# Kernel optimization log

Measured on AMD Instinct MI355X. Metric: run time of the kernel, lower is better.

The kernel has to match this reference:

```python
import jax, jax.numpy as jnp
import numpy as np

ALPHA = 0.2  # LeakyReLU negative slope
NEG_INF = -9e15


def setup_inputs() -> dict:
    key = jax.random.key(0)
    k1, k2, k3, k4, k5 = jax.random.split(key, 5)
    B, N, F_in, F_out = 1, 8192, 256, 128
    h = jax.random.normal(k1, (B, N, F_in), dtype=jnp.float32)
    adj_mat = jax.random.randint(k2, (B, N, N), 0, 2, dtype=jnp.int32)
    W = jax.random.normal(k3, (F_out, F_in), dtype=jnp.float32) * 0.05
    b = jax.random.normal(k4, (F_out,), dtype=jnp.float32) * 0.05
    a = jax.random.normal(k5, (2 * F_out, 1), dtype=jnp.float32) * 0.05
    return {"h": h, "adj_mat": adj_mat, "W": W, "b": b, "a": a}


def reference(h, adj_mat, W, b, a):
    # Wh: (B, N, F_out)
    Wh = jnp.einsum('bnf,of->bno', h, W) + b
    F_out = W.shape[0]
    # Original builds concat[Wh_i, Wh_j] @ a. Equivalent: a1.Wh_i + a2.Wh_j.
    a1 = a[:F_out, 0]
    a2 = a[F_out:, 0]
    s1 = Wh @ a1  # (B, N) source-i contribution
    s2 = Wh @ a2  # (B, N) source-j contribution
    e = s1[:, :, None] + s2[:, None, :]  # (B, N, N)
    e = jnp.where(e >= 0, e, ALPHA * e)  # LeakyReLU
    e = jnp.where(adj_mat > 0, e, NEG_INF)
    attention = jax.nn.softmax(e, axis=1)  # softmax over dim=1, as in the source
    h_prime = jnp.einsum('bij,bjf->bif', attention, Wh)
    return jax.nn.elu(h_prime)
```

## Files before the change

### kernel.cpp

```cpp
#include <hip/hip_runtime.h>

#define NN 8192
#define FI 256
#define FO 128
#define GAT_ALPHA 0.2f

typedef _Float16 f16x8 __attribute__((ext_vector_type(8)));
typedef _Float16 f16x2 __attribute__((ext_vector_type(2)));
typedef float f32x4 __attribute__((ext_vector_type(4)));
typedef unsigned char uchar;
typedef unsigned int uint32;

__global__ __launch_bounds__(256) void k1_wh(const float* __restrict__ h,
                                             const float* __restrict__ W,
                                             const float* __restrict__ bias,
                                             const float* __restrict__ a,
                                             float* __restrict__ Wh,
                                             float4* __restrict__ r4,
                                             float4* __restrict__ c4,
                                             float2* __restrict__ r2,
                                             _Float16* __restrict__ ey16,
                                             _Float16* __restrict__ ez16,
                                             float* __restrict__ s2x,
                                             float* __restrict__ corr) {
  __shared__ float hs[32][FI + 1];
  __shared__ float wt[32][FO];
  const int t = threadIdx.x;
  const int j0 = blockIdx.x * 32;
  if (blockIdx.x == 0 && t < FO) corr[t] = 0.f;
  {
    const int row = t >> 3, c0 = (t & 7) * 32;
    const float* src = h + (size_t)(j0 + row) * FI + c0;
#pragma unroll
    for (int e = 0; e < 8; ++e) {
      float4 v = *(const float4*)(src + 4 * e);
      hs[row][c0 + 4 * e + 0] = v.x;
      hs[row][c0 + 4 * e + 1] = v.y;
      hs[row][c0 + 4 * e + 2] = v.z;
      hs[row][c0 + 4 * e + 3] = v.w;
    }
  }
  const int f4 = (t & 31) * 4;
  const int r0 = (t >> 5) * 4;
  float acc[4][4];
#pragma unroll
  for (int r = 0; r < 4; ++r)
#pragma unroll
    for (int e = 0; e < 4; ++e) acc[r][e] = 0.f;

  for (int kc = 0; kc < FI; kc += 32) {
    __syncthreads();
    {
      const int f = t >> 1, kb = (t & 1) * 16;
      const float* wsrc = W + (size_t)f * FI + kc + kb;
#pragma unroll
      for (int e = 0; e < 16; ++e) wt[kb + e][f] = wsrc[e];
    }
    __syncthreads();
#pragma unroll
    for (int k = 0; k < 32; ++k) {
      const float4 wv = *(const float4*)&wt[k][f4];
      float hv[4];
#pragma unroll
      for (int r = 0; r < 4; ++r) hv[r] = hs[r0 + r][kc + k];
#pragma unroll
      for (int r = 0; r < 4; ++r) {
        acc[r][0] += hv[r] * wv.x;
        acc[r][1] += hv[r] * wv.y;
        acc[r][2] += hv[r] * wv.z;
        acc[r][3] += hv[r] * wv.w;
      }
    }
  }
  const float4 bv = *(const float4*)&bias[f4];
  const float4 a1v = *(const float4*)&a[f4];
  const float4 a2v = *(const float4*)&a[FO + f4];
  float s1p[4], s2p[4];
#pragma unroll
  for (int r = 0; r < 4; ++r) {
    float4 o;
    o.x = acc[r][0] + bv.x;
    o.y = acc[r][1] + bv.y;
    o.z = acc[r][2] + bv.z;
    o.w = acc[r][3] + bv.w;
    *(float4*)&Wh[(size_t)(j0 + r0 + r) * FO + f4] = o;
    s1p[r] = o.x * a1v.x + o.y * a1v.y + o.z * a1v.z + o.w * a1v.w;
    s2p[r] = o.x * a2v.x + o.y * a2v.y + o.z * a2v.z + o.w * a2v.w;
  }
#pragma unroll
  for (int m = 16; m >= 1; m >>= 1) {
#pragma unroll
    for (int r = 0; r < 4; ++r) {
      s1p[r] += __shfl_xor(s1p[r], m);
      s2p[r] += __shfl_xor(s2p[r], m);
    }
  }
  if ((t & 31) == 0) {
#pragma unroll
    for (int r = 0; r < 4; ++r) {
      const int j = j0 + r0 + r;
      const float s1 = s1p[r], s2 = s2p[r];
      const float e1 = expf(s1), e1a = expf(GAT_ALPHA * s1);
      const float e2 = expf(s2), e2a = expf(GAT_ALPHA * s2);
      float4 rv; rv.x = s1; rv.y = e1; rv.z = e1a; rv.w = 0.f;
      float4 cv; cv.x = s2; cv.y = e2; cv.z = e2a; cv.w = 0.f;
      r4[j] = rv;
      c4[j] = cv;
      r2[j] = make_float2(e1, e1a);
      ey16[j] = (_Float16)e2;
      ez16[j] = (_Float16)e2a;
      s2x[j] = s2;
    }
  }
}

__global__ __launch_bounds__(256) void k2_stats(const int* __restrict__ adj,
                                                const float4* __restrict__ r4,
                                                const float* __restrict__ s2x,
                                                uchar* __restrict__ bitsB,
                                                float2* __restrict__ zpart) {
  __shared__ float4 rs[64];
  const int t = threadIdx.x;
  const int jc = blockIdx.x & 3;
  const int ic = blockIdx.x >> 2;
  const int i0 = ic * 64;
  const int j0 = jc * 2048 + t * 8;
  if (t < 64) rs[t] = r4[i0 + t];
  const float4 ca = *(const float4*)(s2x + j0);
  const float4 cb = *(const float4*)(s2x + j0 + 4);
  const float cx[8] = {ca.x, ca.y, ca.z, ca.w, cb.x, cb.y, cb.z, cb.w};
  float accP[8], accN[8];
#pragma unroll
  for (int e = 0; e < 8; ++e) { accP[e] = 0.f; accN[e] = 0.f; }
  __syncthreads();
  const int4* ap = (const int4*)(adj + (size_t)i0 * NN + j0);
  uchar* bp = bitsB + (size_t)i0 * (NN / 8) + jc * 256 + t;
  for (int ir = 0; ir < 64; ir += 8) {
    int4 av[8][2];
#pragma unroll
    for (int u = 0; u < 8; ++u) {
      av[u][0] = ap[(size_t)(ir + u) * (NN / 4)];
      av[u][1] = ap[(size_t)(ir + u) * (NN / 4) + 1];
    }
#pragma unroll
    for (int u = 0; u < 8; ++u) {
      const float4 ri = rs[ir + u];
      const int aa[8] = {av[u][0].x, av[u][0].y, av[u][0].z, av[u][0].w,
                         av[u][1].x, av[u][1].y, av[u][1].z, av[u][1].w};
      uint32 byte = 0;
#pragma unroll
      for (int e = 0; e < 8; ++e) {
        const bool act = aa[e] > 0;
        byte |= act ? (1u << e) : 0u;
        const bool pos = (ri.x + cx[e]) >= 0.f;
        accP[e] += (act && pos) ? ri.y : 0.f;
        accN[e] += (act && !pos) ? ri.z : 0.f;
      }
      bp[(size_t)(ir + u) * (NN / 8)] = (uchar)byte;
    }
  }
  float2* zp = zpart + (size_t)ic * NN + j0;
#pragma unroll
  for (int e = 0; e < 8; ++e) zp[e] = make_float2(accP[e], accN[e]);
}

__global__ __launch_bounds__(256) void k3_scale(const float* __restrict__ Wh,
                                                const float4* __restrict__ c4,
                                                const float2* __restrict__ zpart,
                                                _Float16* __restrict__ Wfrag,
                                                float* __restrict__ corr) {
  __shared__ float rz[64];
  __shared__ int emp[64];
  __shared__ float2 psum[256];
  __shared__ __align__(16) _Float16 tile[FO * 64];
  const int t = threadIdx.x;
  const int j0 = blockIdx.x * 64;
  {
    const int jl = t & 63, q = t >> 6;
    float p = 0.f, n = 0.f;
    for (int ic = q * 32; ic < q * 32 + 32; ++ic) {
      const float2 z = zpart[(size_t)ic * NN + j0 + jl];
      p += z.x;
      n += z.y;
    }
    psum[t] = make_float2(p, n);
  }
  __syncthreads();
  if (t < 64) {
    const float p = psum[t].x + psum[64 + t].x + psum[128 + t].x + psum[192 + t].x;
    const float n = psum[t].y + psum[64 + t].y + psum[128 + t].y + psum[192 + t].y;
    const float4 cj = c4[j0 + t];
    const float Z = cj.y * p + cj.z * n;
    rz[t] = (Z > 0.f) ? 1.f / Z : 0.f;
    emp[t] = (Z > 0.f) ? 0 : 1;
  }
  __syncthreads();
  const int f = t & 127, half = t >> 7;
  const unsigned swf = (unsigned)((f & 7) << 4);
  for (int r = half; r < 64; r += 2) {
    const float v = Wh[(size_t)(j0 + r) * FO + f];
    *(_Float16*)((char*)tile + f * 128 + (((unsigned)(r * 2)) ^ swf)) =
        (_Float16)(v * rz[r]);
    if (emp[r]) atomicAdd(&corr[f], v * (1.f / 8192.f));
  }
  __syncthreads();
#pragma unroll
  for (int q = 0; q < 4; ++q) {
    const int G = t + 256 * q;
    const int kcfb = G >> 6, gl = G & 63;
    const int kc = kcfb >> 3, fb = kcfb & 7;
    const int gf = fb * 16 + (gl & 15);
    const int jloc = kc * 32 + (gl >> 4) * 8;
    const f16x8 v = *(const f16x8*)((const char*)tile + gf * 128 +
                                    (((unsigned)(jloc * 2)) ^ ((unsigned)((gf & 7) << 4))));
    ((f16x8*)Wfrag)[(size_t)(((j0 >> 5) + kc) * 8 + fb) * 64 + gl] = v;
  }
}

#define BARRIER_LDS()                                          \
  do {                                                         \
    __builtin_amdgcn_sched_barrier(0);                         \
    asm volatile("s_waitcnt lgkmcnt(0)" ::: "memory");         \
    __builtin_amdgcn_s_barrier();                              \
    __builtin_amdgcn_sched_barrier(0);                         \
  } while (0)

__global__ __launch_bounds__(256) void k4_main(const uchar* __restrict__ bitsB,
                                               const float2* __restrict__ r2,
                                               const _Float16* __restrict__ ey16,
                                               const _Float16* __restrict__ ez16,
                                               const _Float16* __restrict__ Wfrag,
                                               float* __restrict__ part) {
  __shared__ __align__(16) _Float16 P[2][32 * 64];
  __shared__ uint32 lut[256][4];
  const int t = threadIdx.x;
  const int rowtile = blockIdx.x >> 2;
  const int kq = blockIdx.x & 3;
  const int rowbase = rowtile * 32;
  const int koff = kq * 2048;

  {
#pragma unroll
    for (int p = 0; p < 4; ++p) {
      const uint32 lo = ((t >> (2 * p)) & 1) ? 0x0000FFFFu : 0u;
      const uint32 hi = ((t >> (2 * p + 1)) & 1) ? 0xFFFF0000u : 0u;
      lut[t][p] = lo | hi;
    }
  }

  const int pr = t >> 3, jq = t & 7;
  const float2 rr = r2[rowbase + pr];
  const f16x2 rx2 = {(_Float16)rr.x, (_Float16)rr.x};
  const f16x2 ry2 = {(_Float16)rr.y, (_Float16)rr.y};
  const uchar* bp = bitsB + (size_t)(rowbase + pr) * (NN / 8) + (koff >> 3) + jq;
  const _Float16* eyp = ey16 + koff + jq * 8;
  const _Float16* ezp = ez16 + koff + jq * 8;
  char* const pdst0 = (char*)&P[0][0] + pr * 128 + (((unsigned)(jq * 16)) ^ ((unsigned)((pr & 7) << 4)));
  char* const pdst1 = (char*)&P[1][0] + pr * 128 + (((unsigned)(jq * 16)) ^ ((unsigned)((pr & 7) << 4)));

  const int lane = t & 63, wc = t >> 6;
  const int kgrp = lane >> 4, l15 = lane & 15;
  const unsigned asw = (unsigned)((l15 & 7) << 4);
  const int ar0 = l15 * 128;
  const int ar1 = ar0 + 16 * 128;

  f32x4 acc00 = {0.f, 0.f, 0.f, 0.f}, acc01 = {0.f, 0.f, 0.f, 0.f};
  f32x4 acc10 = {0.f, 0.f, 0.f, 0.f}, acc11 = {0.f, 0.f, 0.f, 0.f};

  uchar mb0, mb1;
  uint4 ey0, ez0, ey1, ez1;
  f16x8 B000, B001, B010, B011, B100, B101, B110, B111;

#define LOADALL(S, MB, EY, EZ, Bq00, Bq01, Bq10, Bq11)                              \
  do {                                                                              \
    MB = bp[(S) * 8];                                                               \
    EY = *(const uint4*)(eyp + (S) * 64);                                           \
    EZ = *(const uint4*)(ezp + (S) * 64);                                           \
    const _Float16* _b = Wfrag + ((size_t)((kq * 64 + (S) * 2) * 8 + wc * 2) * 64 + lane) * 8; \
    Bq00 = *(const f16x8*)(_b);                                                     \
    Bq01 = *(const f16x8*)(_b + 512);                                               \
    Bq10 = *(const f16x8*)(_b + 4096);                                              \
    Bq11 = *(const f16x8*)(_b + 4096 + 512);                                        \
  } while (0)

#define PGEN(DST, MB, EY, EZ)                                                        \
  do {                                                                               \
    const uint4 _m = *(const uint4*)(&lut[MB][0]);                                   \
    const uint32 _eys[4] = {EY.x, EY.y, EY.z, EY.w};                                 \
    const uint32 _ezs[4] = {EZ.x, EZ.y, EZ.z, EZ.w};                                 \
    const uint32 _ms[4] = {_m.x, _m.y, _m.z, _m.w};                                  \
    uint32 _o[4];                                                                    \
    _Pragma("unroll") for (int _p = 0; _p < 4; ++_p) {                               \
      const f16x2 _a = __builtin_bit_cast(f16x2, _eys[_p]) * rx2;                    \
      const f16x2 _b2 = __builtin_bit_cast(f16x2, _ezs[_p]) * ry2;                   \
      const f16x2 _mx = __builtin_elementwise_max(_a, _b2);                          \
      _o[_p] = __builtin_bit_cast(uint32, _mx) & _ms[_p];                            \
    }                                                                                \
    uint4 _st; _st.x = _o[0]; _st.y = _o[1]; _st.z = _o[2]; _st.w = _o[3];           \
    *(uint4*)(DST) = _st;                                                            \
  } while (0)

#define DO_MFMA(BUF, Bq00, Bq01, Bq10, Bq11)                                        \
  do {                                                                              \
    const char* _Pb = (const char*)&P[BUF][0];                                      \
    const f16x8 a00 = *(const f16x8*)(_Pb + ar0 + ((((unsigned)(kgrp * 16))) ^ asw));        \
    const f16x8 a01 = *(const f16x8*)(_Pb + ar0 + (((unsigned)(64 + kgrp * 16)) ^ asw));     \
    const f16x8 a10 = *(const f16x8*)(_Pb + ar1 + ((((unsigned)(kgrp * 16))) ^ asw));        \
    const f16x8 a11 = *(const f16x8*)(_Pb + ar1 + (((unsigned)(64 + kgrp * 16)) ^ asw));     \
    __builtin_amdgcn_s_setprio(1);                                                  \
    acc00 = __builtin_amdgcn_mfma_f32_16x16x32_f16(a00, Bq00, acc00, 0, 0, 0);      \
    acc01 = __builtin_amdgcn_mfma_f32_16x16x32_f16(a00, Bq01, acc01, 0, 0, 0);      \
    acc10 = __builtin_amdgcn_mfma_f32_16x16x32_f16(a10, Bq00, acc10, 0, 0, 0);      \
    acc11 = __builtin_amdgcn_mfma_f32_16x16x32_f16(a10, Bq01, acc11, 0, 0, 0);      \
    acc00 = __builtin_amdgcn_mfma_f32_16x16x32_f16(a01, Bq10, acc00, 0, 0, 0);      \
    acc01 = __builtin_amdgcn_mfma_f32_16x16x32_f16(a01, Bq11, acc01, 0, 0, 0);      \
    acc10 = __builtin_amdgcn_mfma_f32_16x16x32_f16(a11, Bq10, acc10, 0, 0, 0);      \
    acc11 = __builtin_amdgcn_mfma_f32_16x16x32_f16(a11, Bq11, acc11, 0, 0, 0);      \
    __builtin_amdgcn_s_setprio(0);                                                  \
  } while (0)

  LOADALL(0, mb0, ey0, ez0, B000, B001, B010, B011);
  LOADALL(1, mb1, ey1, ez1, B100, B101, B110, B111);
  __syncthreads();
  PGEN(pdst0, mb0, ey0, ez0);
  BARRIER_LDS();

  for (int s = 0; s < 32; s += 2) {
    PGEN(pdst1, mb1, ey1, ez1);
    DO_MFMA(0, B000, B001, B010, B011);
    if (s + 2 < 32) LOADALL(s + 2, mb0, ey0, ez0, B000, B001, B010, B011);
    BARRIER_LDS();
    DO_MFMA(1, B100, B101, B110, B111);
    if (s + 2 < 32) PGEN(pdst0, mb0, ey0, ez0);
    if (s + 3 < 32) LOADALL(s + 3, mb1, ey1, ez1, B100, B101, B110, B111);
    BARRIER_LDS();
  }

#undef LOADALL
#undef PGEN
#undef DO_MFMA

  const int orow = rowbase + kgrp * 4;
  const int ocol = wc * 32 + l15;
  float* aP = part + (size_t)kq * NN * FO + (size_t)orow * FO + ocol;
#pragma unroll
  for (int r = 0; r < 4; ++r) {
    aP[(size_t)r * FO] = acc00[r];
    aP[(size_t)r * FO + 16] = acc01[r];
    aP[(size_t)(16 + r) * FO] = acc10[r];
    aP[(size_t)(16 + r) * FO + 16] = acc11[r];
  }
}

__global__ __launch_bounds__(256) void k5_fin(const float* __restrict__ part,
                                              const float* __restrict__ corr,
                                              float* __restrict__ out) {
  const int idx = blockIdx.x * 256 + threadIdx.x;
  const float4 p0 = ((const float4*)part)[idx];
  const float4 p1 = ((const float4*)(part + (size_t)NN * FO))[idx];
  const float4 p2 = ((const float4*)(part + (size_t)2 * NN * FO))[idx];
  const float4 p3 = ((const float4*)(part + (size_t)3 * NN * FO))[idx];
  const float4 c = ((const float4*)corr)[idx & 31];
  float4 v;
  v.x = p0.x + p1.x + p2.x + p3.x + c.x;
  v.y = p0.y + p1.y + p2.y + p3.y + c.y;
  v.z = p0.z + p1.z + p2.z + p3.z + c.z;
  v.w = p0.w + p1.w + p2.w + p3.w + c.w;
  v.x = (v.x > 0.f) ? v.x : (expf(v.x) - 1.f);
  v.y = (v.y > 0.f) ? v.y : (expf(v.y) - 1.f);
  v.z = (v.z > 0.f) ? v.z : (expf(v.z) - 1.f);
  v.w = (v.w > 0.f) ? v.w : (expf(v.w) - 1.f);
  ((float4*)out)[idx] = v;
}

extern "C" void kernel_launch(void* const* d_in, const int* in_sizes, int n_in,
                              void* d_out, int out_size, void* d_ws, size_t ws_size,
                              hipStream_t stream) {
  const float* h = (const float*)d_in[0];
  const int* adj = (const int*)d_in[1];
  const float* W = (const float*)d_in[2];
  const float* b = (const float*)d_in[3];
  const float* a = (const float*)d_in[4];
  float* out = (float*)d_out;
  char* ws = (char*)d_ws;

  float* Wh = (float*)(ws + 0);
  _Float16* Wfrag = (_Float16*)(ws + 0x400000);
  uchar* bits = (uchar*)(ws + 0x600000);
  float2* zpart = (float2*)(ws + 0xE00000);
  float4* r4 = (float4*)(ws + 0x1600000);
  float4* c4 = (float4*)(ws + 0x1620000);
  float2* r2 = (float2*)(ws + 0x1640000);
  _Float16* ey16 = (_Float16*)(ws + 0x1650000);
  _Float16* ez16 = (_Float16*)(ws + 0x1654000);
  float* s2x = (float*)(ws + 0x1658000);
  float* corr = (float*)(ws + 0x1660000);
  float* part = (float*)(ws + 0x1700000);

  k1_wh<<<NN / 32, 256, 0, stream>>>(h, W, b, a, Wh, r4, c4, r2, ey16, ez16, s2x, corr);
  k2_stats<<<512, 256, 0, stream>>>(adj, r4, s2x, bits, zpart);
  k3_scale<<<NN / 64, 256, 0, stream>>>(Wh, c4, zpart, Wfrag, corr);
  k4_main<<<1024, 256, 0, stream>>>(bits, r2, ey16, ez16, Wfrag, part);
  k5_fin<<<(NN * FO / 4) / 256, 256, 0, stream>>>(part, corr, out);
}
```

Measured before the change: 124.9 us.

## Double k-step per phase in main GAT kernel and vectorize Wh GEMM LDS loads

```diff
diff --git a/kernel.cpp b/kernel.cpp
--- a/kernel.cpp
+++ b/kernel.cpp
@@ -9,6 +9,7 @@
 typedef _Float16 f16x2 __attribute__((ext_vector_type(2)));
 typedef float f32x4 __attribute__((ext_vector_type(4)));
 typedef unsigned char uchar;
+typedef unsigned short ushort16;
 typedef unsigned int uint32;
 
 __global__ __launch_bounds__(256) void k1_wh(const float* __restrict__ h,
@@ -23,8 +24,8 @@
                                              _Float16* __restrict__ ez16,
                                              float* __restrict__ s2x,
                                              float* __restrict__ corr) {
-  __shared__ float hs[32][FI + 1];
-  __shared__ float wt[32][FO];
+  __shared__ __align__(16) float hs[32][260];
+  __shared__ __align__(16) float wt[32][FO];
   const int t = threadIdx.x;
   const int j0 = blockIdx.x * 32;
   if (blockIdx.x == 0 && t < FO) corr[t] = 0.f;
@@ -58,17 +59,18 @@
     }
     __syncthreads();
 #pragma unroll
-    for (int k = 0; k < 32; ++k) {
-      const float4 wv = *(const float4*)&wt[k][f4];
-      float hv[4];
-#pragma unroll
-      for (int r = 0; r < 4; ++r) hv[r] = hs[r0 + r][kc + k];
+    for (int k = 0; k < 32; k += 4) {
+      float4 wv[4], hv[4];
+#pragma unroll
+      for (int i = 0; i < 4; ++i) wv[i] = *(const float4*)&wt[k + i][f4];
+#pragma unroll
+      for (int r = 0; r < 4; ++r) hv[r] = *(const float4*)&hs[r0 + r][kc + k];
 #pragma unroll
       for (int r = 0; r < 4; ++r) {
-        acc[r][0] += hv[r] * wv.x;
-        acc[r][1] += hv[r] * wv.y;
-        acc[r][2] += hv[r] * wv.z;
-        acc[r][3] += hv[r] * wv.w;
+        acc[r][0] += hv[r].x * wv[0].x + hv[r].y * wv[1].x + hv[r].z * wv[2].x + hv[r].w * wv[3].x;
+        acc[r][1] += hv[r].x * wv[0].y + hv[r].y * wv[1].y + hv[r].z * wv[2].y + hv[r].w * wv[3].y;
+        acc[r][2] += hv[r].x * wv[0].z + hv[r].y * wv[1].z + hv[r].z * wv[2].z + hv[r].w * wv[3].z;
+        acc[r][3] += hv[r].x * wv[0].w + hv[r].y * wv[1].w + hv[r].z * wv[2].w + hv[r].w * wv[3].w;
       }
     }
   }
@@ -225,13 +227,13 @@
     __builtin_amdgcn_sched_barrier(0);                         \
   } while (0)
 
-__global__ __launch_bounds__(256) void k4_main(const uchar* __restrict__ bitsB,
-                                               const float2* __restrict__ r2,
-                                               const _Float16* __restrict__ ey16,
-                                               const _Float16* __restrict__ ez16,
-                                               const _Float16* __restrict__ Wfrag,
-                                               float* __restrict__ part) {
-  __shared__ __align__(16) _Float16 P[2][32 * 64];
+__global__ __launch_bounds__(256, 4) void k4_main(const uchar* __restrict__ bitsB,
+                                                  const float2* __restrict__ r2,
+                                                  const _Float16* __restrict__ ey16,
+                                                  const _Float16* __restrict__ ez16,
+                                                  const _Float16* __restrict__ Wfrag,
+                                                  float* __restrict__ part) {
+  __shared__ __align__(16) _Float16 P[2][32 * 128];
   __shared__ uint32 lut[256][4];
   const int t = threadIdx.x;
   const int rowtile = blockIdx.x >> 2;
@@ -252,43 +254,55 @@
   const float2 rr = r2[rowbase + pr];
   const f16x2 rx2 = {(_Float16)rr.x, (_Float16)rr.x};
   const f16x2 ry2 = {(_Float16)rr.y, (_Float16)rr.y};
-  const uchar* bp = bitsB + (size_t)(rowbase + pr) * (NN / 8) + (koff >> 3) + jq;
-  const _Float16* eyp = ey16 + koff + jq * 8;
-  const _Float16* ezp = ez16 + koff + jq * 8;
-  char* const pdst0 = (char*)&P[0][0] + pr * 128 + (((unsigned)(jq * 16)) ^ ((unsigned)((pr & 7) << 4)));
-  char* const pdst1 = (char*)&P[1][0] + pr * 128 + (((unsigned)(jq * 16)) ^ ((unsigned)((pr & 7) << 4)));
+  const uchar* bp = bitsB + (size_t)(rowbase + pr) * (NN / 8) + (koff >> 3) + jq * 2;
+  const _Float16* eyp = ey16 + koff + jq * 16;
+  const _Float16* ezp = ez16 + koff + jq * 16;
+  const unsigned psw = (unsigned)((pr & 7) << 4);
+  char* const prow0 = (char*)&P[0][0] + pr * 256;
+  char* const prow1 = (char*)&P[1][0] + pr * 256;
+  const unsigned off0 = ((unsigned)(jq * 32)) ^ psw;
+  const unsigned off1 = ((unsigned)(jq * 32 + 16)) ^ psw;
 
   const int lane = t & 63, wc = t >> 6;
   const int kgrp = lane >> 4, l15 = lane & 15;
   const unsigned asw = (unsigned)((l15 & 7) << 4);
-  const int ar0 = l15 * 128;
-  const int ar1 = ar0 + 16 * 128;
+  const int ar0 = l15 * 256;
+  const int ar1 = ar0 + 16 * 256;
 
   f32x4 acc00 = {0.f, 0.f, 0.f, 0.f}, acc01 = {0.f, 0.f, 0.f, 0.f};
   f32x4 acc10 = {0.f, 0.f, 0.f, 0.f}, acc11 = {0.f, 0.f, 0.f, 0.f};
 
-  uchar mb0, mb1;
-  uint4 ey0, ez0, ey1, ez1;
-  f16x8 B000, B001, B010, B011, B100, B101, B110, B111;
-
-#define LOADALL(S, MB, EY, EZ, Bq00, Bq01, Bq10, Bq11)                              \
+  ushort16 mb0, mb1;
+  uint4 eya0, eyb0, eza0, ezb0, eya1, eyb1, eza1, ezb1;
+  f16x8 B00, B01, B10, B11, B20, B21, B30, B31;
+
+#define LOADSMALL(PH, MB, EYA, EYB, EZA, EZB)          \
+  do {                                                 \
+    MB = *(const ushort16*)(bp + (PH)*16);             \
+    EYA = *(const uint4*)(eyp + (PH)*128);             \
+    EYB = *(const uint4*)(eyp + (PH)*128 + 8);         \
+    EZA = *(const uint4*)(ezp + (PH)*128);             \
+    EZB = *(const uint4*)(ezp + (PH)*128 + 8);         \
+  } while (0)
+
+#define LOADB(PH)                                                                   \
   do {                                                                              \
-    MB = bp[(S) * 8];                                                               \
-    EY = *(const uint4*)(eyp + (S) * 64);                                           \
-    EZ = *(const uint4*)(ezp + (S) * 64);                                           \
-    const _Float16* _b = Wfrag + ((size_t)((kq * 64 + (S) * 2) * 8 + wc * 2) * 64 + lane) * 8; \
-    Bq00 = *(const f16x8*)(_b);                                                     \
-    Bq01 = *(const f16x8*)(_b + 512);                                               \
-    Bq10 = *(const f16x8*)(_b + 4096);                                              \
-    Bq11 = *(const f16x8*)(_b + 4096 + 512);                                        \
-  } while (0)
-
-#define PGEN(DST, MB, EY, EZ)                                                        \
+    const _Float16* _b = Wfrag + ((size_t)((kq * 64 + (PH)*4) * 8 + wc * 2) * 64 + lane) * 8; \
+    B00 = *(const f16x8*)(_b);                                                      \
+    B01 = *(const f16x8*)(_b + 512);                                                \
+    B10 = *(const f16x8*)(_b + 4096);                                               \
+    B11 = *(const f16x8*)(_b + 4096 + 512);                                         \
+    B20 = *(const f16x8*)(_b + 8192);                                               \
+    B21 = *(const f16x8*)(_b + 8192 + 512);                                         \
+    B30 = *(const f16x8*)(_b + 12288);                                              \
+    B31 = *(const f16x8*)(_b + 12288 + 512);                                        \
+  } while (0)
+
+#define PKHALF(OUT, EY, EZ, MSK)                                                     \
   do {                                                                               \
-    const uint4 _m = *(const uint4*)(&lut[MB][0]);                                   \
     const uint32 _eys[4] = {EY.x, EY.y, EY.z, EY.w};                                 \
     const uint32 _ezs[4] = {EZ.x, EZ.y, EZ.z, EZ.w};                                 \
-    const uint32 _ms[4] = {_m.x, _m.y, _m.z, _m.w};                                  \
+    const uint32 _ms[4] = {MSK.x, MSK.y, MSK.z, MSK.w};                              \
     uint32 _o[4];                                                                    \
     _Pragma("unroll") for (int _p = 0; _p < 4; ++_p) {                               \
       const f16x2 _a = __builtin_bit_cast(f16x2, _eys[_p]) * rx2;                    \
@@ -296,47 +310,74 @@
       const f16x2 _mx = __builtin_elementwise_max(_a, _b2);                          \
       _o[_p] = __builtin_bit_cast(uint32, _mx) & _ms[_p];                            \
     }                                                                                \
-    uint4 _st; _st.x = _o[0]; _st.y = _o[1]; _st.z = _o[2]; _st.w = _o[3];           \
-    *(uint4*)(DST) = _st;                                                            \
-  } while (0)
-
-#define DO_MFMA(BUF, Bq00, Bq01, Bq10, Bq11)                                        \
-  do {                                                                              \
-    const char* _Pb = (const char*)&P[BUF][0];                                      \
-    const f16x8 a00 = *(const f16x8*)(_Pb + ar0 + ((((unsigned)(kgrp * 16))) ^ asw));        \
-    const f16x8 a01 = *(const f16x8*)(_Pb + ar0 + (((unsigned)(64 + kgrp * 16)) ^ asw));     \
-    const f16x8 a10 = *(const f16x8*)(_Pb + ar1 + ((((unsigned)(kgrp * 16))) ^ asw));        \
-    const f16x8 a11 = *(const f16x8*)(_Pb + ar1 + (((unsigned)(64 + kgrp * 16)) ^ asw));     \
-    __builtin_amdgcn_s_setprio(1);                                                  \
-    acc00 = __builtin_amdgcn_mfma_f32_16x16x32_f16(a00, Bq00, acc00, 0, 0, 0);      \
-    acc01 = __builtin_amdgcn_mfma_f32_16x16x32_f16(a00, Bq01, acc01, 0, 0, 0);      \
-    acc10 = __builtin_amdgcn_mfma_f32_16x16x32_f16(a10, Bq00, acc10, 0, 0, 0);      \
-    acc11 = __builtin_amdgcn_mfma_f32_16x16x32_f16(a10, Bq01, acc11, 0, 0, 0);      \
-    acc00 = __builtin_amdgcn_mfma_f32_16x16x32_f16(a01, Bq10, acc00, 0, 0, 0);      \
-    acc01 = __builtin_amdgcn_mfma_f32_16x16x32_f16(a01, Bq11, acc01, 0, 0, 0);      \
-    acc10 = __builtin_amdgcn_mfma_f32_16x16x32_f16(a11, Bq10, acc10, 0, 0, 0);      \
-    acc11 = __builtin_amdgcn_mfma_f32_16x16x32_f16(a11, Bq11, acc11, 0, 0, 0);      \
-    __builtin_amdgcn_s_setprio(0);                                                  \
-  } while (0)
-
-  LOADALL(0, mb0, ey0, ez0, B000, B001, B010, B011);
-  LOADALL(1, mb1, ey1, ez1, B100, B101, B110, B111);
+    OUT.x = _o[0]; OUT.y = _o[1]; OUT.z = _o[2]; OUT.w = _o[3];                      \
+  } while (0)
+
+#define PGEN(PROW, MB, EYA, EYB, EZA, EZB)                                           \
+  do {                                                                               \
+    const uint32 _b0 = (MB) & 0xFF, _b1 = ((MB) >> 8) & 0xFF;                        \
+    const uint4 _m0 = *(const uint4*)(&lut[_b0][0]);                                 \
+    const uint4 _m1 = *(const uint4*)(&lut[_b1][0]);                                 \
+    uint4 _v0, _v1;                                                                  \
+    PKHALF(_v0, EYA, EZA, _m0);                                                      \
+    PKHALF(_v1, EYB, EZB, _m1);                                                      \
+    *(uint4*)(PROW + off0) = _v0;                                                    \
+    *(uint4*)(PROW + off1) = _v1;                                                    \
+  } while (0)
+
+#define DO_MFMA(BUF)                                                                 \
+  do {                                                                               \
+    const char* _Pb = (const char*)&P[BUF][0];                                       \
+    const f16x8 a00 = *(const f16x8*)(_Pb + ar0 + ((((unsigned)(kgrp * 16))) ^ asw));         \
+    const f16x8 a01 = *(const f16x8*)(_Pb + ar0 + (((unsigned)(64 + kgrp * 16)) ^ asw));      \
+    const f16x8 a02 = *(const f16x8*)(_Pb + ar0 + (((unsigned)(128 + kgrp * 16)) ^ asw));     \
+    const f16x8 a03 = *(const f16x8*)(_Pb + ar0 + (((unsigned)(192 + kgrp * 16)) ^ asw));     \
+    const f16x8 a10 = *(const f16x8*)(_Pb + ar1 + ((((unsigned)(kgrp * 16))) ^ asw));         \
+    const f16x8 a11 = *(const f16x8*)(_Pb + ar1 + (((unsigned)(64 + kgrp * 16)) ^ asw));      \
+    const f16x8 a12 = *(const f16x8*)(_Pb + ar1 + (((unsigned)(128 + kgrp * 16)) ^ asw));     \
+    const f16x8 a13 = *(const f16x8*)(_Pb + ar1 + (((unsigned)(192 + kgrp * 16)) ^ asw));     \
+    __builtin_amdgcn_s_setprio(1);                                                   \
+    acc00 = __builtin_amdgcn_mfma_f32_16x16x32_f16(a00, B00, acc00, 0, 0, 0);        \
+    acc01 = __builtin_amdgcn_mfma_f32_16x16x32_f16(a00, B01, acc01, 0, 0, 0);        \
+    acc10 = __builtin_amdgcn_mfma_f32_16x16x32_f16(a10, B00, acc10, 0, 0, 0);        \
+    acc11 = __builtin_amdgcn_mfma_f32_16x16x32_f16(a10, B01, acc11, 0, 0, 0);        \
+    acc00 = __builtin_amdgcn_mfma_f32_16x16x32_f16(a01, B10, acc00, 0, 0, 0);        \
+    acc01 = __builtin_amdgcn_mfma_f32_16x16x32_f16(a01, B11, acc01, 0, 0, 0);        \
+    acc10 = __builtin_amdgcn_mfma_f32_16x16x32_f16(a11, B10, acc10, 0, 0, 0);        \
+    acc11 = __builtin_amdgcn_mfma_f32_16x16x32_f16(a11, B11, acc11, 0, 0, 0);        \
+    acc00 = __builtin_amdgcn_mfma_f32_16x16x32_f16(a02, B20, acc00, 0, 0, 0);        \
+    acc01 = __builtin_amdgcn_mfma_f32_16x16x32_f16(a02, B21, acc01, 0, 0, 0);        \
+    acc10 = __builtin_amdgcn_mfma_f32_16x16x32_f16(a12, B20, acc10, 0, 0, 0);        \
+    acc11 = __builtin_amdgcn_mfma_f32_16x16x32_f16(a12, B21, acc11, 0, 0, 0);        \
+    acc00 = __builtin_amdgcn_mfma_f32_16x16x32_f16(a03, B30, acc00, 0, 0, 0);        \
+    acc01 = __builtin_amdgcn_mfma_f32_16x16x32_f16(a03, B31, acc01, 0, 0, 0);        \
+    acc10 = __builtin_amdgcn_mfma_f32_16x16x32_f16(a13, B30, acc10, 0, 0, 0);        \
+    acc11 = __builtin_amdgcn_mfma_f32_16x16x32_f16(a13, B31, acc11, 0, 0, 0);        \
+    __builtin_amdgcn_s_setprio(0);                                                   \
+  } while (0)
+
+  LOADSMALL(0, mb0, eya0, eyb0, eza0, ezb0);
+  LOADSMALL(1, mb1, eya1, eyb1, eza1, ezb1);
   __syncthreads();
-  PGEN(pdst0, mb0, ey0, ez0);
+  PGEN(prow0, mb0, eya0, eyb0, eza0, ezb0);
   BARRIER_LDS();
 
-  for (int s = 0; s < 32; s += 2) {
-    PGEN(pdst1, mb1, ey1, ez1);
-    DO_MFMA(0, B000, B001, B010, B011);
-    if (s + 2 < 32) LOADALL(s + 2, mb0, ey0, ez0, B000, B001, B010, B011);
+  for (int p = 0; p < 16; p += 2) {
+    LOADB(p);
+    PGEN(prow1, mb1, eya1, eyb1, eza1, ezb1);
+    if (p + 2 < 16) LOADSMALL(p + 2, mb0, eya0, eyb0, eza0, ezb0);
+    DO_MFMA(0);
     BARRIER_LDS();
-    DO_MFMA(1, B100, B101, B110, B111);
-    if (s + 2 < 32) PGEN(pdst0, mb0, ey0, ez0);
-    if (s + 3 < 32) LOADALL(s + 3, mb1, ey1, ez1, B100, B101, B110, B111);
+    LOADB(p + 1);
+    if (p + 2 < 16) PGEN(prow0, mb0, eya0, eyb0, eza0, ezb0);
+    if (p + 3 < 16) LOADSMALL(p + 3, mb1, eya1, eyb1, eza1, ezb1);
+    DO_MFMA(1);
     BARRIER_LDS();
   }
 
-#undef LOADALL
+#undef LOADSMALL
+#undef LOADB
+#undef PKHALF
 #undef PGEN
 #undef DO_MFMA
 
```

Measured after the change: 138.0 us. 1.1x slower.

## Fold normalization into column exp factors and fuse final reduction into main kernel

Applied to the files above, without the earlier changes.

```diff
diff --git a/kernel.cpp b/kernel.cpp
--- a/kernel.cpp
+++ b/kernel.cpp
@@ -19,15 +19,19 @@
                                              float4* __restrict__ r4,
                                              float4* __restrict__ c4,
                                              float2* __restrict__ r2,
-                                             _Float16* __restrict__ ey16,
-                                             _Float16* __restrict__ ez16,
                                              float* __restrict__ s2x,
-                                             float* __restrict__ corr) {
+                                             float* __restrict__ corr,
+                                             uint32* __restrict__ counters,
+                                             _Float16* __restrict__ Wfrag) {
   __shared__ float hs[32][FI + 1];
-  __shared__ float wt[32][FO];
+  __shared__ __align__(16) float wt[32][FO];
+  _Float16* const tileb = (_Float16*)&wt[0][0];
   const int t = threadIdx.x;
   const int j0 = blockIdx.x * 32;
-  if (blockIdx.x == 0 && t < FO) corr[t] = 0.f;
+  if (blockIdx.x == 0) {
+    if (t < FO) corr[t] = 0.f;
+    counters[t] = 0u;
+  }
   {
     const int row = t >> 3, c0 = (t & 7) * 32;
     const float* src = h + (size_t)(j0 + row) * FI + c0;
@@ -72,6 +76,7 @@
       }
     }
   }
+  __syncthreads();
   const float4 bv = *(const float4*)&bias[f4];
   const float4 a1v = *(const float4*)&a[f4];
   const float4 a2v = *(const float4*)&a[FO + f4];
@@ -84,6 +89,14 @@
     o.z = acc[r][2] + bv.z;
     o.w = acc[r][3] + bv.w;
     *(float4*)&Wh[(size_t)(j0 + r0 + r) * FO + f4] = o;
+    const int jloc = r0 + r;
+    const float ov[4] = {o.x, o.y, o.z, o.w};
+#pragma unroll
+    for (int e = 0; e < 4; ++e) {
+      const int gf = f4 + e;
+      *(_Float16*)((char*)tileb + gf * 64 + (((unsigned)(jloc * 2)) ^ ((unsigned)(e << 4)))) =
+          (_Float16)ov[e];
+    }
     s1p[r] = o.x * a1v.x + o.y * a1v.y + o.z * a1v.z + o.w * a1v.w;
     s2p[r] = o.x * a2v.x + o.y * a2v.y + o.z * a2v.z + o.w * a2v.w;
   }
@@ -107,10 +120,19 @@
       r4[j] = rv;
       c4[j] = cv;
       r2[j] = make_float2(e1, e1a);
-      ey16[j] = (_Float16)e2;
-      ez16[j] = (_Float16)e2a;
       s2x[j] = s2;
     }
+  }
+  __syncthreads();
+#pragma unroll
+  for (int q = 0; q < 2; ++q) {
+    const int G = t + 256 * q;
+    const int fb = G >> 6, gl = G & 63;
+    const int gf = fb * 16 + (gl & 15);
+    const int jloc = (gl >> 4) * 8;
+    const f16x8 v = *(const f16x8*)((const char*)tileb + gf * 64 +
+                                    (((unsigned)(jloc * 2)) ^ ((unsigned)((gf & 3) << 4))));
+    ((f16x8*)Wfrag)[(size_t)(blockIdx.x * 8 + fb) * 64 + gl] = v;
   }
 }
 
@@ -164,56 +186,28 @@
   for (int e = 0; e < 8; ++e) zp[e] = make_float2(accP[e], accN[e]);
 }
 
-__global__ __launch_bounds__(256) void k3_scale(const float* __restrict__ Wh,
-                                                const float4* __restrict__ c4,
-                                                const float2* __restrict__ zpart,
-                                                _Float16* __restrict__ Wfrag,
-                                                float* __restrict__ corr) {
-  __shared__ float rz[64];
-  __shared__ int emp[64];
-  __shared__ float2 psum[256];
-  __shared__ __align__(16) _Float16 tile[FO * 64];
-  const int t = threadIdx.x;
-  const int j0 = blockIdx.x * 64;
-  {
-    const int jl = t & 63, q = t >> 6;
-    float p = 0.f, n = 0.f;
-    for (int ic = q * 32; ic < q * 32 + 32; ++ic) {
-      const float2 z = zpart[(size_t)ic * NN + j0 + jl];
-      p += z.x;
-      n += z.y;
-    }
-    psum[t] = make_float2(p, n);
-  }
-  __syncthreads();
-  if (t < 64) {
-    const float p = psum[t].x + psum[64 + t].x + psum[128 + t].x + psum[192 + t].x;
-    const float n = psum[t].y + psum[64 + t].y + psum[128 + t].y + psum[192 + t].y;
-    const float4 cj = c4[j0 + t];
-    const float Z = cj.y * p + cj.z * n;
-    rz[t] = (Z > 0.f) ? 1.f / Z : 0.f;
-    emp[t] = (Z > 0.f) ? 0 : 1;
-  }
-  __syncthreads();
-  const int f = t & 127, half = t >> 7;
-  const unsigned swf = (unsigned)((f & 7) << 4);
-  for (int r = half; r < 64; r += 2) {
-    const float v = Wh[(size_t)(j0 + r) * FO + f];
-    *(_Float16*)((char*)tile + f * 128 + (((unsigned)(r * 2)) ^ swf)) =
-        (_Float16)(v * rz[r]);
-    if (emp[r]) atomicAdd(&corr[f], v * (1.f / 8192.f));
-  }
-  __syncthreads();
-#pragma unroll
-  for (int q = 0; q < 4; ++q) {
-    const int G = t + 256 * q;
-    const int kcfb = G >> 6, gl = G & 63;
-    const int kc = kcfb >> 3, fb = kcfb & 7;
-    const int gf = fb * 16 + (gl & 15);
-    const int jloc = kc * 32 + (gl >> 4) * 8;
-    const f16x8 v = *(const f16x8*)((const char*)tile + gf * 128 +
-                                    (((unsigned)(jloc * 2)) ^ ((unsigned)((gf & 7) << 4))));
-    ((f16x8*)Wfrag)[(size_t)(((j0 >> 5) + kc) * 8 + fb) * 64 + gl] = v;
+__global__ __launch_bounds__(256) void k3_rz(const float4* __restrict__ c4,
+                                             const float2* __restrict__ zpart,
+                                             const float* __restrict__ Wh,
+                                             _Float16* __restrict__ ey16,
+                                             _Float16* __restrict__ ez16,
+                                             float* __restrict__ corr) {
+  const int j = blockIdx.x * 256 + threadIdx.x;
+  float p = 0.f, n = 0.f;
+#pragma unroll 8
+  for (int ic = 0; ic < 128; ++ic) {
+    const float2 z = zpart[(size_t)ic * NN + j];
+    p += z.x;
+    n += z.y;
+  }
+  const float4 cj = c4[j];
+  const float Z = cj.y * p + cj.z * n;
+  const float rz = (Z > 0.f) ? 1.f / Z : 0.f;
+  ey16[j] = (_Float16)(cj.y * rz);
+  ez16[j] = (_Float16)(cj.z * rz);
+  if (!(Z > 0.f)) {
+    const float* wr = Wh + (size_t)j * FO;
+    for (int f = 0; f < FO; ++f) atomicAdd(&corr[f], wr[f] * (1.f / 8192.f));
   }
 }
 
@@ -230,9 +224,13 @@
                                                const _Float16* __restrict__ ey16,
                                                const _Float16* __restrict__ ez16,
                                                const _Float16* __restrict__ Wfrag,
-                                               float* __restrict__ part) {
+                                               float* __restrict__ part,
+                                               const float* __restrict__ corr,
+                                               uint32* __restrict__ counters,
+                                               float* __restrict__ out) {
   __shared__ __align__(16) _Float16 P[2][32 * 64];
   __shared__ uint32 lut[256][4];
+  __shared__ uint32 lastflag;
   const int t = threadIdx.x;
   const int rowtile = blockIdx.x >> 2;
   const int kq = blockIdx.x & 3;
@@ -350,27 +348,35 @@
     aP[(size_t)(16 + r) * FO] = acc10[r];
     aP[(size_t)(16 + r) * FO + 16] = acc11[r];
   }
-}
-
-__global__ __launch_bounds__(256) void k5_fin(const float* __restrict__ part,
-                                              const float* __restrict__ corr,
-                                              float* __restrict__ out) {
-  const int idx = blockIdx.x * 256 + threadIdx.x;
-  const float4 p0 = ((const float4*)part)[idx];
-  const float4 p1 = ((const float4*)(part + (size_t)NN * FO))[idx];
-  const float4 p2 = ((const float4*)(part + (size_t)2 * NN * FO))[idx];
-  const float4 p3 = ((const float4*)(part + (size_t)3 * NN * FO))[idx];
-  const float4 c = ((const float4*)corr)[idx & 31];
-  float4 v;
-  v.x = p0.x + p1.x + p2.x + p3.x + c.x;
-  v.y = p0.y + p1.y + p2.y + p3.y + c.y;
-  v.z = p0.z + p1.z + p2.z + p3.z + c.z;
-  v.w = p0.w + p1.w + p2.w + p3.w + c.w;
-  v.x = (v.x > 0.f) ? v.x : (expf(v.x) - 1.f);
-  v.y = (v.y > 0.f) ? v.y : (expf(v.y) - 1.f);
-  v.z = (v.z > 0.f) ? v.z : (expf(v.z) - 1.f);
-  v.w = (v.w > 0.f) ? v.w : (expf(v.w) - 1.f);
-  ((float4*)out)[idx] = v;
+
+  __threadfence();
+  if (t == 0) lastflag = (atomicAdd(&counters[rowtile], 1u) == 3u) ? 1u : 0u;
+  __syncthreads();
+  if (lastflag) {
+    __threadfence();
+    const float c0 = corr[ocol];
+    const float c1 = corr[ocol + 16];
+#pragma unroll
+    for (int r = 0; r < 4; ++r) {
+      float v00 = c0, v01 = c1, v10 = c0, v11 = c1;
+#pragma unroll
+      for (int q = 0; q < 4; ++q) {
+        const float* pp = part + (size_t)q * NN * FO;
+        v00 += pp[(size_t)(orow + r) * FO + ocol];
+        v01 += pp[(size_t)(orow + r) * FO + ocol + 16];
+        v10 += pp[(size_t)(orow + 16 + r) * FO + ocol];
+        v11 += pp[(size_t)(orow + 16 + r) * FO + ocol + 16];
+      }
+      v00 = (v00 > 0.f) ? v00 : (expf(v00) - 1.f);
+      v01 = (v01 > 0.f) ? v01 : (expf(v01) - 1.f);
+      v10 = (v10 > 0.f) ? v10 : (expf(v10) - 1.f);
+      v11 = (v11 > 0.f) ? v11 : (expf(v11) - 1.f);
+      out[(size_t)(orow + r) * FO + ocol] = v00;
+      out[(size_t)(orow + r) * FO + ocol + 16] = v01;
+      out[(size_t)(orow + 16 + r) * FO + ocol] = v10;
+      out[(size_t)(orow + 16 + r) * FO + ocol + 16] = v11;
+    }
+  }
 }
 
 extern "C" void kernel_launch(void* const* d_in, const int* in_sizes, int n_in,
@@ -395,11 +401,11 @@
   _Float16* ez16 = (_Float16*)(ws + 0x1654000);
   float* s2x = (float*)(ws + 0x1658000);
   float* corr = (float*)(ws + 0x1660000);
+  uint32* counters = (uint32*)(ws + 0x1661000);
   float* part = (float*)(ws + 0x1700000);
 
-  k1_wh<<<NN / 32, 256, 0, stream>>>(h, W, b, a, Wh, r4, c4, r2, ey16, ez16, s2x, corr);
+  k1_wh<<<NN / 32, 256, 0, stream>>>(h, W, b, a, Wh, r4, c4, r2, s2x, corr, counters, Wfrag);
   k2_stats<<<512, 256, 0, stream>>>(adj, r4, s2x, bits, zpart);
-  k3_scale<<<NN / 64, 256, 0, stream>>>(Wh, c4, zpart, Wfrag, corr);
-  k4_main<<<1024, 256, 0, stream>>>(bits, r2, ey16, ez16, Wfrag, part);
-  k5_fin<<<(NN * FO / 4) / 256, 256, 0, stream>>>(part, corr, out);
+  k3_rz<<<32, 256, 0, stream>>>(c4, zpart, Wh, ey16, ez16, corr);
+  k4_main<<<1024, 256, 0, stream>>>(bits, r2, ey16, ez16, Wfrag, part, corr, counters, out);
 }
```

Measured after the change: 312.5 us. +150.3%, slower.
